# Optimization experiments

Measured on AMD Instinct MI355X. Metric: run time of the kernel, lower is better.

Reference implementation:

```python
import jax, jax.numpy as jnp
import numpy as np

NUM_USERS = 100000
NUM_ITEMS = 20000
DIM = 64
NUM_TAG = 64
NUM_NEG = 8
B = 262144
M_IMP = 2000
MARGIN1 = 0.1
MARGIN2 = 0.1
LAMBDA1 = 1.0
LAMBDA2 = 1.0
TAU = 0.2
EPS = 1e-7
MAX_NORM = 1.0 - 1e-5


def _norm(x, keepdims=True):
    return jnp.sqrt(jnp.maximum(jnp.sum(x * x, -1, keepdims=keepdims), 1e-15))


def artanh(x):
    x = jnp.clip(x, -MAX_NORM, MAX_NORM)
    return 0.5 * (jnp.log1p(x) - jnp.log1p(-x))


def acosh(z):
    z = jnp.maximum(z, 1.0 + EPS)
    return jnp.log(z + jnp.sqrt(z * z - 1.0))


# ---- Poincare ball, c = 1 ----
def ball_projx(x):
    n = _norm(x)
    return jnp.where(n > MAX_NORM, x * (MAX_NORM / n), x)


def ball_expmap0(u):
    n = _norm(u)
    return jnp.tanh(n) * u / n


def ball_logmap0(x):
    n = _norm(x)
    return artanh(n) * x / n


def mobius_add(x, y):
    xy = jnp.sum(x * y, -1, keepdims=True)
    x2 = jnp.sum(x * x, -1, keepdims=True)
    y2 = jnp.sum(y * y, -1, keepdims=True)
    num = (1.0 + 2.0 * xy + y2) * x + (1.0 - x2) * y
    den = 1.0 + 2.0 * xy + x2 * y2
    return num / jnp.maximum(den, 1e-15)


def mobius_matvec(w, x):
    # x: [..., in], w: [out, in] -> mx = x @ w.T (geoopt convention)
    mx = x @ w.T
    xn = _norm(x)
    mn = _norm(mx)
    return jnp.tanh(mn / xn * artanh(xn)) * mx / mn


def ball_dist2(x, y):
    d = 2.0 * artanh(_norm(mobius_add(-x, y), keepdims=False))
    return d * d


# ---- Lorentz, k = 1 ----
def lorentz_dist2(x, y):
    inner = jnp.sum(x[..., 1:] * y[..., 1:], -1) - x[..., 0] * y[..., 0]
    d = acosh(-inner)
    return d * d


def setup_inputs() -> dict:
    key = jax.random.key(0)
    ks = jax.random.split(key, 10)
    # Lorentz points (k=1): x0 = sqrt(1 + ||x_spatial||^2)
    sp = jax.random.normal(ks[0], (NUM_USERS + NUM_ITEMS, DIM - 1), jnp.float32) * 0.5
    t = jnp.sqrt(1.0 + jnp.sum(sp * sp, -1, keepdims=True))
    embeddings = jnp.concatenate([t, sp], -1)
    vtg_weight = jax.random.normal(ks[1], (NUM_ITEMS, DIM), jnp.float32) * 0.01
    emb_tag = ball_expmap0(jax.random.normal(ks[2], (NUM_TAG, DIM), jnp.float32) * 0.1)
    kk = (6.0 / (2 * DIM)) ** 0.5
    lin_weight = jax.random.uniform(ks[3], (DIM, DIM), jnp.float32, -kk, kk)
    lin_bias = ball_expmap0(jax.random.normal(ks[4], (DIM,), jnp.float32) * 0.001)
    tag_weight = jnp.zeros((NUM_TAG,), jnp.float32)
    uu = jax.random.randint(ks[5], (B, 1), 0, NUM_USERS)
    it = jax.random.randint(ks[6], (B, 1 + NUM_NEG), NUM_USERS, NUM_USERS + NUM_ITEMS)
    triples = jnp.concatenate([uu, it], 1)
    tag_labels = jax.random.randint(ks[7], (NUM_ITEMS, NUM_TAG), 0, 2)
    a = jax.random.randint(ks[8], (M_IMP,), 0, NUM_TAG)
    b = (a + 1 + jax.random.randint(ks[9], (M_IMP,), 0, NUM_TAG - 1)) % NUM_TAG
    implication = jnp.stack([a, b], 1)
    return dict(embeddings=embeddings, vtg_weight=vtg_weight, emb_tag=emb_tag,
                lin_weight=lin_weight, lin_bias=lin_bias, tag_weight=tag_weight,
                triples=triples, tag_labels=tag_labels, implication=implication)


def reference(embeddings, vtg_weight, emb_tag, lin_weight, lin_bias, tag_weight,
              triples, tag_labels, implication):
    # ---- hyperbolic margin-ranking loss ----
    u = embeddings[triples[:, 0]]                         # [B, D]
    pos = embeddings[triples[:, 1]]                       # [B, D]
    neg = embeddings[triples[:, 2:]]                      # [B, NEG, D]
    pos_scores = lorentz_dist2(u, pos)[:, None]           # [B, 1]
    neg_scores = lorentz_dist2(u[:, None, :], neg)        # [B, NEG]
    # alpha = sqrt(dist2(u, origin)) = acosh(u0) for Lorentz k=1
    alpha = acosh(u[:, 0])[:, None]
    rank_loss = jnp.sum(jnp.maximum((pos_scores - neg_scores + MARGIN2) * alpha, 0.0))

    # ---- Ex_loss: MobiusLinear then tangent-space cdist ----
    enc = ball_projx(vtg_weight)
    h = mobius_matvec(lin_weight, enc)
    h = ball_projx(mobius_add(h, lin_bias[None, :]))
    a = ball_logmap0(h)                                   # [I, D]
    bt = ball_logmap0(emb_tag)                            # [T, D]
    sq = jnp.sum(a * a, -1)[:, None] + jnp.sum(bt * bt, -1)[None, :] - 2.0 * a @ bt.T
    dist = jnp.sqrt(jnp.maximum(sq, 1e-12))
    logits = dist / jnp.exp(tag_weight)[None, :]          # [I, T]
    logp = jnp.log(logits)
    # relu(log(target) - log(all_dist) + margin1) summed over all tags,
    # masked to the positive-tag positions (== np.where(tag_labels>0) gather)
    term = jnp.maximum(logp[:, :, None] - logp[:, None, :] + MARGIN1, 0.0)  # [I, T, T]
    mask = (tag_labels > 0).astype(logp.dtype)
    cls_loss = jnp.sum(term.sum(-1) * mask)

    # ---- tag-hierarchy contrastive loss ----
    q = emb_tag[implication[:, 0]]
    p = emb_tag[implication[:, 1]]
    dist_pos = ball_dist2(q, p)[:, None]                               # [M, 1]
    dist_neg = ball_dist2(q[:, None, :], emb_tag[None, :, :])          # [M, T]
    full = jnp.concatenate([dist_pos, dist_neg], 1)                    # [M, T+1]
    # original filters out entries <= 1e-9 (the self-distance zero); masking
    # them to -inf in logit space is the permutation-invariant equivalent
    cl_logits = jnp.where(full > 1e-9, -full / TAU, -1e30)
    cl_loss = jnp.sum(jax.nn.logsumexp(cl_logits, axis=1) + dist_pos[:, 0] / TAU)

    return rank_loss + LAMBDA1 * cls_loss + LAMBDA2 * cl_loss
```

## Files before the change

### kernel.cpp

```cpp
#include <hip/hip_runtime.h>
#include <math.h>

namespace {

constexpr int NUM_NEG   = 8;
constexpr int BROWS     = 262144;
constexpr float MARGIN1 = 0.1f;
constexpr float MARGIN2 = 0.1f;
constexpr float TAU     = 0.2f;
constexpr float EPS1    = 1e-7f;
constexpr float MAXNORM = 1.0f - 1e-5f;

constexpr int RANK_BLOCKS = 4096;
constexpr int RANK_WAVES  = RANK_BLOCKS * 4;
constexpr int CLS_BLOCKS  = 2500;
constexpr int CLS_WAVES   = CLS_BLOCKS * 4;
constexpr int CL_BLOCKS   = 500;
constexpr int NBLK = RANK_BLOCKS + CLS_BLOCKS + CL_BLOCKS;

typedef __attribute__((ext_vector_type(4))) float f32x4;

__device__ __forceinline__ float wredsum(float v) {
    v += __shfl_xor(v, 1);  v += __shfl_xor(v, 2);  v += __shfl_xor(v, 4);
    v += __shfl_xor(v, 8);  v += __shfl_xor(v, 16); v += __shfl_xor(v, 32);
    return v;
}
__device__ __forceinline__ void wredsum2(float& a, float& b) {
    a += __shfl_xor(a, 1);  b += __shfl_xor(b, 1);
    a += __shfl_xor(a, 2);  b += __shfl_xor(b, 2);
    a += __shfl_xor(a, 4);  b += __shfl_xor(b, 4);
    a += __shfl_xor(a, 8);  b += __shfl_xor(b, 8);
    a += __shfl_xor(a, 16); b += __shfl_xor(b, 16);
    a += __shfl_xor(a, 32); b += __shfl_xor(b, 32);
}
__device__ __forceinline__ void wredsum4(float& a, float& b, float& c, float& d) {
    a += __shfl_xor(a, 1);  b += __shfl_xor(b, 1);
    c += __shfl_xor(c, 1);  d += __shfl_xor(d, 1);
    a += __shfl_xor(a, 2);  b += __shfl_xor(b, 2);
    c += __shfl_xor(c, 2);  d += __shfl_xor(d, 2);
    a += __shfl_xor(a, 4);  b += __shfl_xor(b, 4);
    c += __shfl_xor(c, 4);  d += __shfl_xor(d, 4);
    a += __shfl_xor(a, 8);  b += __shfl_xor(b, 8);
    c += __shfl_xor(c, 8);  d += __shfl_xor(d, 8);
    a += __shfl_xor(a, 16); b += __shfl_xor(b, 16);
    c += __shfl_xor(c, 16); d += __shfl_xor(d, 16);
    a += __shfl_xor(a, 32); b += __shfl_xor(b, 32);
    c += __shfl_xor(c, 32); d += __shfl_xor(d, 32);
}
__device__ __forceinline__ float wredmax(float v) {
    v = fmaxf(v, __shfl_xor(v, 1));  v = fmaxf(v, __shfl_xor(v, 2));
    v = fmaxf(v, __shfl_xor(v, 4));  v = fmaxf(v, __shfl_xor(v, 8));
    v = fmaxf(v, __shfl_xor(v, 16)); v = fmaxf(v, __shfl_xor(v, 32));
    return v;
}
__device__ __forceinline__ float bcast(float v, int l) {
    return __int_as_float(__builtin_amdgcn_readlane(__float_as_int(v), l));
}
__device__ __forceinline__ float fsq(float x)  { return __builtin_amdgcn_sqrtf(x); }
__device__ __forceinline__ float frc(float x)  { return __builtin_amdgcn_rcpf(x); }
__device__ __forceinline__ float artanh_fast(float n) {
    n = fminf(n, MAXNORM);
    return 0.5f * __logf((1.f + n) * frc(1.f - n));
}
__device__ __forceinline__ float acosh_fast(float z) {
    z = fmaxf(z, 1.0f + EPS1);
    return __logf(z + fsq(fmaf(z, z, -1.0f)));
}
__device__ __forceinline__ float tanh_fast(float x) {
    const float t = __expf(2.f * x);
    return (t - 1.f) * frc(t + 1.f);
}
__device__ __forceinline__ float dot4(const f32x4& a, const f32x4& b) {
    return (a.x * b.x + a.y * b.y) + (a.z * b.z + a.w * b.w);
}

__global__ __launch_bounds__(256) void fused_kernel(
        const float* __restrict__ emb,  const int* __restrict__ tri,
        const float* __restrict__ vtg,  const float* __restrict__ etag,
        const float* __restrict__ linw, const float* __restrict__ linb,
        const float* __restrict__ tw,   const int* __restrict__ labels,
        const int* __restrict__ imp,    float* __restrict__ part) {
    __shared__ float SA[64 * 65];
    __shared__ float XS[4 * 128];
    __shared__ float s64v[64];
    __shared__ float red4[4];
    const int tid  = threadIdx.x;
    const int lane = tid & 63, wid = tid >> 6;
    const int b    = blockIdx.x;
    float wsum = 0.f;

    const int rb  = (int)(((long)b       * RANK_BLOCKS) / NBLK);
    const int rb1 = (int)(((long)(b + 1) * RANK_BLOCKS) / NBLK);
    const bool is_rank = (rb1 > rb);
    const int  o = b - rb;

    if (is_rank) {
        const int gw  = rb * 4 + wid;
        const int sub = lane & 7;
        const int rw  = lane >> 3;
        const int dof = sub * 8;
        const bool o0 = sub & 1;
        const bool o1 = (sub >> 1) & 1;
        const bool o2 = (sub >> 2) & 1;
        float racc = 0.f;

        const int  row0 = gw * 8 + rw;
        const int* t0 = tri + (long)row0 * 10;
        const int* t1 = t0 + (long)(RANK_WAVES * 8) * 10;
        const int2 a01 = *reinterpret_cast<const int2*>(t0);
        const int2 a23 = *reinterpret_cast<const int2*>(t0 + 2);
        const int2 a45 = *reinterpret_cast<const int2*>(t0 + 4);
        const int2 a67 = *reinterpret_cast<const int2*>(t0 + 6);
        const int2 a89 = *reinterpret_cast<const int2*>(t0 + 8);
        const int2 b01 = *reinterpret_cast<const int2*>(t1);
        const int2 b23 = *reinterpret_cast<const int2*>(t1 + 2);
        const int2 b45 = *reinterpret_cast<const int2*>(t1 + 4);
        const int2 b67 = *reinterpret_cast<const int2*>(t1 + 6);
        const int2 b89 = *reinterpret_cast<const int2*>(t1 + 8);

        auto ldvec = [&](int idx, f32x4& lo, f32x4& hi) {
            const float* q = emb + (long)idx * 64 + dof;
            lo = *reinterpret_cast<const f32x4*>(q);
            hi = *reinterpret_cast<const f32x4*>(q + 4);
        };
        auto finish = [&](float e0, float e1, float e2, float e3,
                          float e4, float e5, float e6, float e7,
                          float ps, float alpha) {
            float s_;
            s_ = o0 ? e0 : e1; s_ = __shfl_xor(s_, 1); const float f0 = (o0 ? e1 : e0) + s_;
            s_ = o0 ? e2 : e3; s_ = __shfl_xor(s_, 1); const float f1 = (o0 ? e3 : e2) + s_;
            s_ = o0 ? e4 : e5; s_ = __shfl_xor(s_, 1); const float f2 = (o0 ? e5 : e4) + s_;
            s_ = o0 ? e6 : e7; s_ = __shfl_xor(s_, 1); const float f3 = (o0 ? e7 : e6) + s_;
            s_ = o1 ? f0 : f1; s_ = __shfl_xor(s_, 2); const float g0 = (o1 ? f1 : f0) + s_;
            s_ = o1 ? f2 : f3; s_ = __shfl_xor(s_, 2); const float g1 = (o1 ? f3 : f2) + s_;
            s_ = o2 ? g0 : g1; s_ = __shfl_xor(s_, 4); const float dn = (o2 ? g1 : g0) + s_;
            const float dneg = acosh_fast(-dn);
            racc += alpha * fmaxf(ps - dneg * dneg + MARGIN2, 0.f);
        };

        f32x4 ua0, ub0, pa0, pb0;
        f32x4 na0,nb0, na1,nb1, na2,nb2, na3,nb3, na4,nb4, na5,nb5, na6,nb6, na7,nb7;
        ldvec(a01.x, ua0, ub0);  ldvec(a01.y, pa0, pb0);
        ldvec(a23.x, na0, nb0);  ldvec(a23.y, na1, nb1);
        ldvec(a45.x, na2, nb2);  ldvec(a45.y, na3, nb3);
        ldvec(a67.x, na4, nb4);  ldvec(a67.y, na5, nb5);
        ldvec(a89.x, na6, nb6);  ldvec(a89.y, na7, nb7);
        asm volatile(""
            : "+v"(ua0), "+v"(ub0), "+v"(pa0), "+v"(pb0),
              "+v"(na0), "+v"(nb0), "+v"(na1), "+v"(nb1),
              "+v"(na2), "+v"(nb2), "+v"(na3), "+v"(nb3),
              "+v"(na4), "+v"(nb4), "+v"(na5), "+v"(nb5),
              "+v"(na6), "+v"(nb6), "+v"(na7), "+v"(nb7));

        const float u00  = ua0.x;
        const float u0b0 = __shfl(u00, lane & 56);
        if (sub == 0) ua0.x = -ua0.x;
        float dp0 = dot4(ua0, pa0) + dot4(ub0, pb0);
        dp0 += __shfl_xor(dp0, 1); dp0 += __shfl_xor(dp0, 2); dp0 += __shfl_xor(dp0, 4);
        const float dpos0  = acosh_fast(-dp0);
        const float ps0    = dpos0 * dpos0;
        const float alpha0 = acosh_fast(u0b0);
        const float e0 = dot4(ua0, na0) + dot4(ub0, nb0);
        const float e1 = dot4(ua0, na1) + dot4(ub0, nb1);
        const float e2 = dot4(ua0, na2) + dot4(ub0, nb2);
        const float e3 = dot4(ua0, na3) + dot4(ub0, nb3);
        const float e4 = dot4(ua0, na4) + dot4(ub0, nb4);
        const float e5 = dot4(ua0, na5) + dot4(ub0, nb5);
        const float e6 = dot4(ua0, na6) + dot4(ub0, nb6);
        const float e7 = dot4(ua0, na7) + dot4(ub0, nb7);
        finish(e0, e1, e2, e3, e4, e5, e6, e7, ps0, alpha0);

        f32x4 ua1, ub1, pa1, pb1;
        f32x4 qa0,qb0, qa1,qb1, qa2,qb2, qa3,qb3, qa4,qb4, qa5,qb5, qa6,qb6, qa7,qb7;
        ldvec(b01.x, ua1, ub1);  ldvec(b01.y, pa1, pb1);
        ldvec(b23.x, qa0, qb0);  ldvec(b23.y, qa1, qb1);
        ldvec(b45.x, qa2, qb2);  ldvec(b45.y, qa3, qb3);
        ldvec(b67.x, qa4, qb4);  ldvec(b67.y, qa5, qb5);
        ldvec(b89.x, qa6, qb6);  ldvec(b89.y, qa7, qb7);
        asm volatile(""
            : "+v"(ua1), "+v"(ub1), "+v"(pa1), "+v"(pb1),
              "+v"(qa0), "+v"(qb0), "+v"(qa1), "+v"(qb1),
              "+v"(qa2), "+v"(qb2), "+v"(qa3), "+v"(qb3),
              "+v"(qa4), "+v"(qb4), "+v"(qa5), "+v"(qb5),
              "+v"(qa6), "+v"(qb6), "+v"(qa7), "+v"(qb7));

        const float u01  = ua1.x;
        const float u0b1 = __shfl(u01, lane & 56);
        if (sub == 0) ua1.x = -ua1.x;
        float dp1 = dot4(ua1, pa1) + dot4(ub1, pb1);
        dp1 += __shfl_xor(dp1, 1); dp1 += __shfl_xor(dp1, 2); dp1 += __shfl_xor(dp1, 4);
        const float dpos1  = acosh_fast(-dp1);
        const float ps1    = dpos1 * dpos1;
        const float alpha1 = acosh_fast(u0b1);
        const float h0 = dot4(ua1, qa0) + dot4(ub1, qb0);
        const float h1 = dot4(ua1, qa1) + dot4(ub1, qb1);
        const float h2 = dot4(ua1, qa2) + dot4(ub1, qb2);
        const float h3 = dot4(ua1, qa3) + dot4(ub1, qb3);
        const float h4 = dot4(ua1, qa4) + dot4(ub1, qb4);
        const float h5 = dot4(ua1, qa5) + dot4(ub1, qb5);
        const float h6 = dot4(ua1, qa6) + dot4(ub1, qb6);
        const float h7 = dot4(ua1, qa7) + dot4(ub1, qb7);
        finish(h0, h1, h2, h3, h4, h5, h6, h7, ps1, alpha1);

        wsum = wredsum(racc);
    } else if (o < CLS_BLOCKS) {
        const int gw = o * 4 + wid;
        const int i0 = gw, i1 = gw + CLS_WAVES;
        const int xb = wid * 128;

        for (int i = tid; i < 4096; i += 256) {
            SA[(i & 63) * 65 + (i >> 6)] = linw[i];
        }
        __syncthreads();
        const float bias = linb[lane];
        const float y2b  = wredsum(bias * bias);

        float xv0 = vtg[(long)i0 * 64 + lane];
        float xv1 = vtg[(long)i1 * 64 + lane];
        float n20 = xv0 * xv0, n21 = xv1 * xv1;
        wredsum2(n20, n21);
        float xn0 = fsq(fmaxf(n20, 1e-15f)), xn1 = fsq(fmaxf(n21, 1e-15f));
        if (xn0 > MAXNORM) { xv0 *= MAXNORM * frc(xn0); float t = wredsum(xv0 * xv0); xn0 = fsq(fmaxf(t, 1e-15f)); }
        if (xn1 > MAXNORM) { xv1 *= MAXNORM * frc(xn1); float t = wredsum(xv1 * xv1); xn1 = fsq(fmaxf(t, 1e-15f)); }

        XS[xb + lane]      = xv0;
        XS[xb + 64 + lane] = xv1;
        float ma0 = 0.f, ma1 = 0.f, mb0 = 0.f, mb1 = 0.f;
        #pragma unroll
        for (int d = 0; d < 64; d += 2) {
            const float w0 = SA[(d)     * 65 + lane];
            const float w1 = SA[(d + 1) * 65 + lane];
            const float xA0 = XS[xb + d],      xA1 = XS[xb + d + 1];
            const float xB0 = XS[xb + 64 + d], xB1 = XS[xb + 64 + d + 1];
            ma0 = fmaf(xA0, w0, ma0);  ma1 = fmaf(xA1, w1, ma1);
            mb0 = fmaf(xB0, w0, mb0);  mb1 = fmaf(xB1, w1, mb1);
        }
        const float mxA = ma0 + ma1, mxB = mb0 + mb1;

        float mnA2 = mxA * mxA, mnB2 = mxB * mxB;
        wredsum2(mnA2, mnB2);
        const float mnA = fsq(fmaxf(mnA2, 1e-15f)), mnB = fsq(fmaxf(mnB2, 1e-15f));
        const float gA = tanh_fast(mnA * frc(xn0) * artanh_fast(xn0));
        const float gB = tanh_fast(mnB * frc(xn1) * artanh_fast(xn1));
        const float hA = gA * frc(mnA) * mxA, hB = gB * frc(mnB) * mxB;
        float x2hA = hA * hA, xyA = hA * bias, x2hB = hB * hB, xyB = hB * bias;
        wredsum4(x2hA, xyA, x2hB, xyB);
        const float AA  = 1.f + 2.f * xyA + y2b, AB = 1.f + 2.f * xyB + y2b;
        const float BcA = 1.f - x2hA,            BcB = 1.f - x2hB;
        const float denA = fmaxf(1.f + 2.f * xyA + x2hA * y2b, 1e-15f);
        const float denB = fmaxf(1.f + 2.f * xyB + x2hB * y2b, 1e-15f);
        float hhA = (AA * hA + BcA * bias) * frc(denA);
        float hhB = (AB * hB + BcB * bias) * frc(denB);
        float h2A = hhA * hhA, h2B = hhB * hhB;
        wredsum2(h2A, h2B);
        float hnA = fsq(fmaxf(h2A, 1e-15f)), hnB = fsq(fmaxf(h2B, 1e-15f));
        if (hnA > MAXNORM) { hhA *= MAXNORM * frc(hnA); float t = wredsum(hhA * hhA); hnA = fsq(fmaxf(t, 1e-15f)); }
        if (hnB > MAXNORM) { hhB *= MAXNORM * frc(hnB); float t = wredsum(hhB * hhB); hnB = fsq(fmaxf(t, 1e-15f)); }
        const float aA = artanh_fast(hnA) * frc(hnA) * hhA;
        const float aB = artanh_fast(hnB) * frc(hnB) * hhB;

        XS[xb + lane]      = aA;
        XS[xb + 64 + lane] = aB;
        __syncthreads();
        {
            const int j = tid >> 2, p = tid & 3;
            float e[16]; float s2 = 0.f;
            #pragma unroll
            for (int m = 0; m < 16; ++m) { e[m] = etag[j * 64 + p * 16 + m]; s2 += e[m] * e[m]; }
            s2 += __shfl_xor(s2, 1); s2 += __shfl_xor(s2, 2);
            const float n  = fsq(fmaxf(s2, 1e-15f));
            const float sc = artanh_fast(n) * frc(n);
            #pragma unroll
            for (int m = 0; m < 16; ++m) SA[(p * 16 + m) * 65 + j] = sc * e[m];
            if (p == 0) s64v[j] = sc * sc * s2;
        }
        __syncthreads();

        float da0 = 0.f, da1 = 0.f, db0 = 0.f, db1 = 0.f;
        #pragma unroll
        for (int d = 0; d < 64; d += 2) {
            const float w0 = SA[(d)     * 65 + lane];
            const float w1 = SA[(d + 1) * 65 + lane];
            const float xA0 = XS[xb + d],      xA1 = XS[xb + d + 1];
            const float xB0 = XS[xb + 64 + d], xB1 = XS[xb + 64 + d + 1];
            da0 = fmaf(xA0, w0, da0);  da1 = fmaf(xA1, w1, da1);
            db0 = fmaf(xB0, w0, db0);  db1 = fmaf(xB1, w1, db1);
        }
        float a2A = aA * aA, a2B = aB * aB;
        wredsum2(a2A, a2B);
        const float b2l = s64v[lane];
        const float twl = tw[lane];
        const float distA = fsq(fmaxf(a2A + b2l - 2.f * (da0 + da1), 1e-12f));
        const float distB = fsq(fmaxf(a2B + b2l - 2.f * (db0 + db1), 1e-12f));
        const float lpA = __logf(distA) - twl;
        const float lpB = __logf(distB) - twl;

        XS[xb + lane]      = lpA;
        XS[xb + 64 + lane] = lpB;
        const float qA = lpA + MARGIN1, qB = lpB + MARGIN1;
        float s00 = 0.f, s01 = 0.f, s10 = 0.f, s11 = 0.f;
        #pragma unroll
        for (int k = 0; k < 64; k += 2) {
            const float lA0 = XS[xb + k],      lA1 = XS[xb + k + 1];
            const float lB0 = XS[xb + 64 + k], lB1 = XS[xb + 64 + k + 1];
            s00 += fmaxf(qA - lA0, 0.f);  s01 += fmaxf(qA - lA1, 0.f);
            s10 += fmaxf(qB - lB0, 0.f);  s11 += fmaxf(qB - lB1, 0.f);
        }
        const float hsA = s00 + s01, hsB = s10 + s11;
        const float cA = (labels[(long)i0 * 64 + lane] > 0) ? hsA : 0.f;
        const float cB = (labels[(long)i1 * 64 + lane] > 0) ? hsB : 0.f;
        wsum = wredsum(cA + cB);
    } else {
        const int gw = (o - CLS_BLOCKS) * 4 + wid;
        {
            const int j = tid >> 2, p = tid & 3;
            float s2 = 0.f;
            #pragma unroll
            for (int m = 0; m < 16; ++m) {
                const float e = etag[j * 64 + p * 16 + m];
                s2 += e * e;
                SA[(p * 16 + m) * 65 + j] = e;
            }
            s2 += __shfl_xor(s2, 1); s2 += __shfl_xor(s2, 2);
            if (p == 0) s64v[j] = s2;
        }
        __syncthreads();
        const int ai = imp[gw * 2];
        const int bi = imp[gw * 2 + 1];
        const float y2l = s64v[lane];
        const float x2  = s64v[ai];
        float c0 = 0.f, c1 = 0.f, c2 = 0.f, c3 = 0.f;
        #pragma unroll
        for (int d = 0; d < 64; d += 4) {
            c0 = fmaf(SA[(d)     * 65 + ai], SA[(d)     * 65 + lane], c0);
            c1 = fmaf(SA[(d + 1) * 65 + ai], SA[(d + 1) * 65 + lane], c1);
            c2 = fmaf(SA[(d + 2) * 65 + ai], SA[(d + 2) * 65 + lane], c2);
            c3 = fmaf(SA[(d + 3) * 65 + ai], SA[(d + 3) * 65 + lane], c3);
        }
        const float c   = (c0 + c1) + (c2 + c3);
        const float A   = 1.f - 2.f * c + y2l;
        const float Bc  = 1.f - x2;
        const float nn  = A * A * x2 - 2.f * A * Bc * c + Bc * Bc * y2l;
        const float den = fmaxf(1.f - 2.f * c + x2 * y2l, 1e-15f);
        float n = fsq(fmaxf(nn * frc(den * den), 1e-15f));
        n = fminf(n, MAXNORM);
        const float dd = __logf((1.f + n) * frc(1.f - n));
        float dist = dd * dd;
        if (lane == ai) dist = 0.f;
        const float logit = (dist > 1e-9f) ? (-dist * (1.f / TAU)) : -1e30f;
        const float dp = bcast(dist, bi);
        const float lp = bcast(logit, bi);
        const float m  = wredmax(logit);
        const float se = wredsum(__expf(logit - m)) + __expf(lp - m);
        wsum = m + __logf(se) + dp * (1.f / TAU);
    }

    if (lane == 0) red4[wid] = wsum;
    __syncthreads();
    if (tid == 0) part[b] = red4[0] + red4[1] + red4[2] + red4[3];
}

__global__ __launch_bounds__(256) void final_reduce(
        const float* __restrict__ parts, int n, float* __restrict__ out) {
    __shared__ double red[256];
    double s = 0.0;
    for (int i = threadIdx.x; i < n; i += 256) s += (double)parts[i];
    red[threadIdx.x] = s;
    __syncthreads();
    for (int off = 128; off > 0; off >>= 1) {
        if (threadIdx.x < off) red[threadIdx.x] += red[threadIdx.x + off];
        __syncthreads();
    }
    if (threadIdx.x == 0) out[0] = (float)red[0];
}

}

extern "C" void kernel_launch(void* const* d_in, const int* in_sizes, int n_in,
                              void* d_out, int out_size, void* d_ws, size_t ws_size,
                              hipStream_t stream) {
    const float* emb    = (const float*)d_in[0];
    const float* vtg    = (const float*)d_in[1];
    const float* etag   = (const float*)d_in[2];
    const float* linw   = (const float*)d_in[3];
    const float* linb   = (const float*)d_in[4];
    const float* tw     = (const float*)d_in[5];
    const int*   tri    = (const int*)d_in[6];
    const int*   labels = (const int*)d_in[7];
    const int*   imp    = (const int*)d_in[8];
    float* parts = (float*)d_ws;

    fused_kernel<<<NBLK, 256, 0, stream>>>(emb, tri, vtg, etag, linw, linb,
                                           tw, labels, imp, parts);
    final_reduce<<<1, 256, 0, stream>>>(parts, NBLK, (float*)d_out);
}
```

Baseline: 72.22 us.

## Cut grid size fourfold with per-wave loops over more rows in each branch

Shrinks the rank, classification and contrastive block counts by a factor of four. Each wave now loops over 8 rank rows (instead of 2), 8 item rows (instead of 2) and 4 implication pairs (instead of 1). This amortizes per-block setup, such as loading weight matrices into shared memory and the tag tables, and reduces the number of partial sums. The cost is fewer blocks, which means less parallelism and latency hiding for the gather-heavy rank section, plus a longer serial dependency chain per wave.

```diff
diff --git a/kernel.cpp b/kernel.cpp
--- a/kernel.cpp
+++ b/kernel.cpp
@@ -11,11 +11,13 @@
 constexpr float EPS1    = 1e-7f;
 constexpr float MAXNORM = 1.0f - 1e-5f;
 
-constexpr int RANK_BLOCKS = 4096;
+constexpr int RANK_BLOCKS = 1024;
 constexpr int RANK_WAVES  = RANK_BLOCKS * 4;
-constexpr int CLS_BLOCKS  = 2500;
+constexpr int RANK_SWEEPS = 8;
+constexpr int CLS_BLOCKS  = 625;
 constexpr int CLS_WAVES   = CLS_BLOCKS * 4;
-constexpr int CL_BLOCKS   = 500;
+constexpr int CL_BLOCKS   = 125;
+constexpr int CL_WAVES    = CL_BLOCKS * 4;
 constexpr int NBLK = RANK_BLOCKS + CLS_BLOCKS + CL_BLOCKS;
 
 typedef __attribute__((ext_vector_type(4))) float f32x4;
@@ -102,30 +104,55 @@
         const bool o0 = sub & 1;
         const bool o1 = (sub >> 1) & 1;
         const bool o2 = (sub >> 2) & 1;
+        const int row0 = gw * 8 + rw;
         float racc = 0.f;
-
-        const int  row0 = gw * 8 + rw;
-        const int* t0 = tri + (long)row0 * 10;
-        const int* t1 = t0 + (long)(RANK_WAVES * 8) * 10;
-        const int2 a01 = *reinterpret_cast<const int2*>(t0);
-        const int2 a23 = *reinterpret_cast<const int2*>(t0 + 2);
-        const int2 a45 = *reinterpret_cast<const int2*>(t0 + 4);
-        const int2 a67 = *reinterpret_cast<const int2*>(t0 + 6);
-        const int2 a89 = *reinterpret_cast<const int2*>(t0 + 8);
-        const int2 b01 = *reinterpret_cast<const int2*>(t1);
-        const int2 b23 = *reinterpret_cast<const int2*>(t1 + 2);
-        const int2 b45 = *reinterpret_cast<const int2*>(t1 + 4);
-        const int2 b67 = *reinterpret_cast<const int2*>(t1 + 6);
-        const int2 b89 = *reinterpret_cast<const int2*>(t1 + 8);
 
         auto ldvec = [&](int idx, f32x4& lo, f32x4& hi) {
             const float* q = emb + (long)idx * 64 + dof;
             lo = *reinterpret_cast<const f32x4*>(q);
             hi = *reinterpret_cast<const f32x4*>(q + 4);
         };
-        auto finish = [&](float e0, float e1, float e2, float e3,
-                          float e4, float e5, float e6, float e7,
-                          float ps, float alpha) {
+
+        #pragma unroll 2
+        for (int s = 0; s < RANK_SWEEPS; ++s) {
+            const int* t = tri + (long)(row0 + s * (RANK_WAVES * 8)) * 10;
+            const int2 a01 = *reinterpret_cast<const int2*>(t);
+            const int2 a23 = *reinterpret_cast<const int2*>(t + 2);
+            const int2 a45 = *reinterpret_cast<const int2*>(t + 4);
+            const int2 a67 = *reinterpret_cast<const int2*>(t + 6);
+            const int2 a89 = *reinterpret_cast<const int2*>(t + 8);
+
+            f32x4 ua, ub, pa, pb;
+            f32x4 na0,nb0, na1,nb1, na2,nb2, na3,nb3,
+                  na4,nb4, na5,nb5, na6,nb6, na7,nb7;
+            ldvec(a01.x, ua, ub);    ldvec(a01.y, pa, pb);
+            ldvec(a23.x, na0, nb0);  ldvec(a23.y, na1, nb1);
+            ldvec(a45.x, na2, nb2);  ldvec(a45.y, na3, nb3);
+            ldvec(a67.x, na4, nb4);  ldvec(a67.y, na5, nb5);
+            ldvec(a89.x, na6, nb6);  ldvec(a89.y, na7, nb7);
+            asm volatile(""
+                : "+v"(ua), "+v"(ub), "+v"(pa), "+v"(pb),
+                  "+v"(na0), "+v"(nb0), "+v"(na1), "+v"(nb1),
+                  "+v"(na2), "+v"(nb2), "+v"(na3), "+v"(nb3),
+                  "+v"(na4), "+v"(nb4), "+v"(na5), "+v"(nb5),
+                  "+v"(na6), "+v"(nb6), "+v"(na7), "+v"(nb7));
+
+            const float u0  = ua.x;
+            const float u0b = __shfl(u0, lane & 56);
+            if (sub == 0) ua.x = -ua.x;
+            float dp = dot4(ua, pa) + dot4(ub, pb);
+            dp += __shfl_xor(dp, 1); dp += __shfl_xor(dp, 2); dp += __shfl_xor(dp, 4);
+            const float dpos  = acosh_fast(-dp);
+            const float ps    = dpos * dpos;
+            const float alpha = acosh_fast(u0b);
+            const float e0 = dot4(ua, na0) + dot4(ub, nb0);
+            const float e1 = dot4(ua, na1) + dot4(ub, nb1);
+            const float e2 = dot4(ua, na2) + dot4(ub, nb2);
+            const float e3 = dot4(ua, na3) + dot4(ub, nb3);
+            const float e4 = dot4(ua, na4) + dot4(ub, nb4);
+            const float e5 = dot4(ua, na5) + dot4(ub, nb5);
+            const float e6 = dot4(ua, na6) + dot4(ub, nb6);
+            const float e7 = dot4(ua, na7) + dot4(ub, nb7);
             float s_;
             s_ = o0 ? e0 : e1; s_ = __shfl_xor(s_, 1); const float f0 = (o0 ? e1 : e0) + s_;
             s_ = o0 ? e2 : e3; s_ = __shfl_xor(s_, 1); const float f1 = (o0 ? e3 : e2) + s_;
@@ -136,76 +163,10 @@
             s_ = o2 ? g0 : g1; s_ = __shfl_xor(s_, 4); const float dn = (o2 ? g1 : g0) + s_;
             const float dneg = acosh_fast(-dn);
             racc += alpha * fmaxf(ps - dneg * dneg + MARGIN2, 0.f);
-        };
-
-        f32x4 ua0, ub0, pa0, pb0;
-        f32x4 na0,nb0, na1,nb1, na2,nb2, na3,nb3, na4,nb4, na5,nb5, na6,nb6, na7,nb7;
-        ldvec(a01.x, ua0, ub0);  ldvec(a01.y, pa0, pb0);
-        ldvec(a23.x, na0, nb0);  ldvec(a23.y, na1, nb1);
-        ldvec(a45.x, na2, nb2);  ldvec(a45.y, na3, nb3);
-        ldvec(a67.x, na4, nb4);  ldvec(a67.y, na5, nb5);
-        ldvec(a89.x, na6, nb6);  ldvec(a89.y, na7, nb7);
-        asm volatile(""
-            : "+v"(ua0), "+v"(ub0), "+v"(pa0), "+v"(pb0),
-              "+v"(na0), "+v"(nb0), "+v"(na1), "+v"(nb1),
-              "+v"(na2), "+v"(nb2), "+v"(na3), "+v"(nb3),
-              "+v"(na4), "+v"(nb4), "+v"(na5), "+v"(nb5),
-              "+v"(na6), "+v"(nb6), "+v"(na7), "+v"(nb7));
-
-        const float u00  = ua0.x;
-        const float u0b0 = __shfl(u00, lane & 56);
-        if (sub == 0) ua0.x = -ua0.x;
-        float dp0 = dot4(ua0, pa0) + dot4(ub0, pb0);
-        dp0 += __shfl_xor(dp0, 1); dp0 += __shfl_xor(dp0, 2); dp0 += __shfl_xor(dp0, 4);
-        const float dpos0  = acosh_fast(-dp0);
-        const float ps0    = dpos0 * dpos0;
-        const float alpha0 = acosh_fast(u0b0);
-        const float e0 = dot4(ua0, na0) + dot4(ub0, nb0);
-        const float e1 = dot4(ua0, na1) + dot4(ub0, nb1);
-        const float e2 = dot4(ua0, na2) + dot4(ub0, nb2);
-        const float e3 = dot4(ua0, na3) + dot4(ub0, nb3);
-        const float e4 = dot4(ua0, na4) + dot4(ub0, nb4);
-        const float e5 = dot4(ua0, na5) + dot4(ub0, nb5);
-        const float e6 = dot4(ua0, na6) + dot4(ub0, nb6);
-        const float e7 = dot4(ua0, na7) + dot4(ub0, nb7);
-        finish(e0, e1, e2, e3, e4, e5, e6, e7, ps0, alpha0);
-
-        f32x4 ua1, ub1, pa1, pb1;
-        f32x4 qa0,qb0, qa1,qb1, qa2,qb2, qa3,qb3, qa4,qb4, qa5,qb5, qa6,qb6, qa7,qb7;
-        ldvec(b01.x, ua1, ub1);  ldvec(b01.y, pa1, pb1);
-        ldvec(b23.x, qa0, qb0);  ldvec(b23.y, qa1, qb1);
-        ldvec(b45.x, qa2, qb2);  ldvec(b45.y, qa3, qb3);
-        ldvec(b67.x, qa4, qb4);  ldvec(b67.y, qa5, qb5);
-        ldvec(b89.x, qa6, qb6);  ldvec(b89.y, qa7, qb7);
-        asm volatile(""
-            : "+v"(ua1), "+v"(ub1), "+v"(pa1), "+v"(pb1),
-              "+v"(qa0), "+v"(qb0), "+v"(qa1), "+v"(qb1),
-              "+v"(qa2), "+v"(qb2), "+v"(qa3), "+v"(qb3),
-              "+v"(qa4), "+v"(qb4), "+v"(qa5), "+v"(qb5),
-              "+v"(qa6), "+v"(qb6), "+v"(qa7), "+v"(qb7));
-
-        const float u01  = ua1.x;
-        const float u0b1 = __shfl(u01, lane & 56);
-        if (sub == 0) ua1.x = -ua1.x;
-        float dp1 = dot4(ua1, pa1) + dot4(ub1, pb1);
-        dp1 += __shfl_xor(dp1, 1); dp1 += __shfl_xor(dp1, 2); dp1 += __shfl_xor(dp1, 4);
-        const float dpos1  = acosh_fast(-dp1);
-        const float ps1    = dpos1 * dpos1;
-        const float alpha1 = acosh_fast(u0b1);
-        const float h0 = dot4(ua1, qa0) + dot4(ub1, qb0);
-        const float h1 = dot4(ua1, qa1) + dot4(ub1, qb1);
-        const float h2 = dot4(ua1, qa2) + dot4(ub1, qb2);
-        const float h3 = dot4(ua1, qa3) + dot4(ub1, qb3);
-        const float h4 = dot4(ua1, qa4) + dot4(ub1, qb4);
-        const float h5 = dot4(ua1, qa5) + dot4(ub1, qb5);
-        const float h6 = dot4(ua1, qa6) + dot4(ub1, qb6);
-        const float h7 = dot4(ua1, qa7) + dot4(ub1, qb7);
-        finish(h0, h1, h2, h3, h4, h5, h6, h7, ps1, alpha1);
-
+        }
         wsum = wredsum(racc);
     } else if (o < CLS_BLOCKS) {
         const int gw = o * 4 + wid;
-        const int i0 = gw, i1 = gw + CLS_WAVES;
         const int xb = wid * 128;
 
         for (int i = tid; i < 4096; i += 256) {
@@ -215,52 +176,54 @@
         const float bias = linb[lane];
         const float y2b  = wredsum(bias * bias);
 
-        float xv0 = vtg[(long)i0 * 64 + lane];
-        float xv1 = vtg[(long)i1 * 64 + lane];
-        float n20 = xv0 * xv0, n21 = xv1 * xv1;
-        wredsum2(n20, n21);
-        float xn0 = fsq(fmaxf(n20, 1e-15f)), xn1 = fsq(fmaxf(n21, 1e-15f));
-        if (xn0 > MAXNORM) { xv0 *= MAXNORM * frc(xn0); float t = wredsum(xv0 * xv0); xn0 = fsq(fmaxf(t, 1e-15f)); }
-        if (xn1 > MAXNORM) { xv1 *= MAXNORM * frc(xn1); float t = wredsum(xv1 * xv1); xn1 = fsq(fmaxf(t, 1e-15f)); }
-
-        XS[xb + lane]      = xv0;
-        XS[xb + 64 + lane] = xv1;
-        float ma0 = 0.f, ma1 = 0.f, mb0 = 0.f, mb1 = 0.f;
-        #pragma unroll
-        for (int d = 0; d < 64; d += 2) {
-            const float w0 = SA[(d)     * 65 + lane];
-            const float w1 = SA[(d + 1) * 65 + lane];
-            const float xA0 = XS[xb + d],      xA1 = XS[xb + d + 1];
-            const float xB0 = XS[xb + 64 + d], xB1 = XS[xb + 64 + d + 1];
-            ma0 = fmaf(xA0, w0, ma0);  ma1 = fmaf(xA1, w1, ma1);
-            mb0 = fmaf(xB0, w0, mb0);  mb1 = fmaf(xB1, w1, mb1);
-        }
-        const float mxA = ma0 + ma1, mxB = mb0 + mb1;
-
-        float mnA2 = mxA * mxA, mnB2 = mxB * mxB;
-        wredsum2(mnA2, mnB2);
-        const float mnA = fsq(fmaxf(mnA2, 1e-15f)), mnB = fsq(fmaxf(mnB2, 1e-15f));
-        const float gA = tanh_fast(mnA * frc(xn0) * artanh_fast(xn0));
-        const float gB = tanh_fast(mnB * frc(xn1) * artanh_fast(xn1));
-        const float hA = gA * frc(mnA) * mxA, hB = gB * frc(mnB) * mxB;
-        float x2hA = hA * hA, xyA = hA * bias, x2hB = hB * hB, xyB = hB * bias;
-        wredsum4(x2hA, xyA, x2hB, xyB);
-        const float AA  = 1.f + 2.f * xyA + y2b, AB = 1.f + 2.f * xyB + y2b;
-        const float BcA = 1.f - x2hA,            BcB = 1.f - x2hB;
-        const float denA = fmaxf(1.f + 2.f * xyA + x2hA * y2b, 1e-15f);
-        const float denB = fmaxf(1.f + 2.f * xyB + x2hB * y2b, 1e-15f);
-        float hhA = (AA * hA + BcA * bias) * frc(denA);
-        float hhB = (AB * hB + BcB * bias) * frc(denB);
-        float h2A = hhA * hhA, h2B = hhB * hhB;
-        wredsum2(h2A, h2B);
-        float hnA = fsq(fmaxf(h2A, 1e-15f)), hnB = fsq(fmaxf(h2B, 1e-15f));
-        if (hnA > MAXNORM) { hhA *= MAXNORM * frc(hnA); float t = wredsum(hhA * hhA); hnA = fsq(fmaxf(t, 1e-15f)); }
-        if (hnB > MAXNORM) { hhB *= MAXNORM * frc(hnB); float t = wredsum(hhB * hhB); hnB = fsq(fmaxf(t, 1e-15f)); }
-        const float aA = artanh_fast(hnA) * frc(hnA) * hhA;
-        const float aB = artanh_fast(hnB) * frc(hnB) * hhB;
-
-        XS[xb + lane]      = aA;
-        XS[xb + 64 + lane] = aB;
+        auto p1pair = [&](int iA, int iB, float& outA, float& outB) {
+            float xv0 = vtg[(long)iA * 64 + lane];
+            float xv1 = vtg[(long)iB * 64 + lane];
+            float n20 = xv0 * xv0, n21 = xv1 * xv1;
+            wredsum2(n20, n21);
+            float xn0 = fsq(fmaxf(n20, 1e-15f)), xn1 = fsq(fmaxf(n21, 1e-15f));
+            if (xn0 > MAXNORM) { xv0 *= MAXNORM * frc(xn0); float t = wredsum(xv0 * xv0); xn0 = fsq(fmaxf(t, 1e-15f)); }
+            if (xn1 > MAXNORM) { xv1 *= MAXNORM * frc(xn1); float t = wredsum(xv1 * xv1); xn1 = fsq(fmaxf(t, 1e-15f)); }
+            XS[xb + lane]      = xv0;
+            XS[xb + 64 + lane] = xv1;
+            float ma0 = 0.f, ma1 = 0.f, mb0 = 0.f, mb1 = 0.f;
+            #pragma unroll
+            for (int d = 0; d < 64; d += 2) {
+                const float w0 = SA[(d)     * 65 + lane];
+                const float w1 = SA[(d + 1) * 65 + lane];
+                const float xA0 = XS[xb + d],      xA1 = XS[xb + d + 1];
+                const float xB0 = XS[xb + 64 + d], xB1 = XS[xb + 64 + d + 1];
+                ma0 = fmaf(xA0, w0, ma0);  ma1 = fmaf(xA1, w1, ma1);
+                mb0 = fmaf(xB0, w0, mb0);  mb1 = fmaf(xB1, w1, mb1);
+            }
+            const float mxA = ma0 + ma1, mxB = mb0 + mb1;
+            float mnA2 = mxA * mxA, mnB2 = mxB * mxB;
+            wredsum2(mnA2, mnB2);
+            const float mnA = fsq(fmaxf(mnA2, 1e-15f)), mnB = fsq(fmaxf(mnB2, 1e-15f));
+            const float gA = tanh_fast(mnA * frc(xn0) * artanh_fast(xn0));
+            const float gB = tanh_fast(mnB * frc(xn1) * artanh_fast(xn1));
+            const float hA = gA * frc(mnA) * mxA, hB = gB * frc(mnB) * mxB;
+            float x2hA = hA * hA, xyA = hA * bias, x2hB = hB * hB, xyB = hB * bias;
+            wredsum4(x2hA, xyA, x2hB, xyB);
+            const float AA  = 1.f + 2.f * xyA + y2b, AB = 1.f + 2.f * xyB + y2b;
+            const float BcA = 1.f - x2hA,            BcB = 1.f - x2hB;
+            const float denA = fmaxf(1.f + 2.f * xyA + x2hA * y2b, 1e-15f);
+            const float denB = fmaxf(1.f + 2.f * xyB + x2hB * y2b, 1e-15f);
+            float hhA = (AA * hA + BcA * bias) * frc(denA);
+            float hhB = (AB * hB + BcB * bias) * frc(denB);
+            float h2A = hhA * hhA, h2B = hhB * hhB;
+            wredsum2(h2A, h2B);
+            float hnA = fsq(fmaxf(h2A, 1e-15f)), hnB = fsq(fmaxf(h2B, 1e-15f));
+            if (hnA > MAXNORM) { hhA *= MAXNORM * frc(hnA); float t = wredsum(hhA * hhA); hnA = fsq(fmaxf(t, 1e-15f)); }
+            if (hnB > MAXNORM) { hhB *= MAXNORM * frc(hnB); float t = wredsum(hhB * hhB); hnB = fsq(fmaxf(t, 1e-15f)); }
+            outA = artanh_fast(hnA) * frc(hnA) * hhA;
+            outB = artanh_fast(hnB) * frc(hnB) * hhB;
+        };
+        float av0, av1, av2, av3, av4, av5, av6, av7;
+        p1pair(gw,                 gw + CLS_WAVES,     av0, av1);
+        p1pair(gw + 2 * CLS_WAVES, gw + 3 * CLS_WAVES, av2, av3);
+        p1pair(gw + 4 * CLS_WAVES, gw + 5 * CLS_WAVES, av4, av5);
+        p1pair(gw + 6 * CLS_WAVES, gw + 7 * CLS_WAVES, av6, av7);
         __syncthreads();
         {
             const int j = tid >> 2, p = tid & 3;
@@ -275,41 +238,50 @@
             if (p == 0) s64v[j] = sc * sc * s2;
         }
         __syncthreads();
-
-        float da0 = 0.f, da1 = 0.f, db0 = 0.f, db1 = 0.f;
-        #pragma unroll
-        for (int d = 0; d < 64; d += 2) {
-            const float w0 = SA[(d)     * 65 + lane];
-            const float w1 = SA[(d + 1) * 65 + lane];
-            const float xA0 = XS[xb + d],      xA1 = XS[xb + d + 1];
-            const float xB0 = XS[xb + 64 + d], xB1 = XS[xb + 64 + d + 1];
-            da0 = fmaf(xA0, w0, da0);  da1 = fmaf(xA1, w1, da1);
-            db0 = fmaf(xB0, w0, db0);  db1 = fmaf(xB1, w1, db1);
-        }
-        float a2A = aA * aA, a2B = aB * aB;
-        wredsum2(a2A, a2B);
         const float b2l = s64v[lane];
         const float twl = tw[lane];
-        const float distA = fsq(fmaxf(a2A + b2l - 2.f * (da0 + da1), 1e-12f));
-        const float distB = fsq(fmaxf(a2B + b2l - 2.f * (db0 + db1), 1e-12f));
-        const float lpA = __logf(distA) - twl;
-        const float lpB = __logf(distB) - twl;
-
-        XS[xb + lane]      = lpA;
-        XS[xb + 64 + lane] = lpB;
-        const float qA = lpA + MARGIN1, qB = lpB + MARGIN1;
-        float s00 = 0.f, s01 = 0.f, s10 = 0.f, s11 = 0.f;
-        #pragma unroll
-        for (int k = 0; k < 64; k += 2) {
-            const float lA0 = XS[xb + k],      lA1 = XS[xb + k + 1];
-            const float lB0 = XS[xb + 64 + k], lB1 = XS[xb + 64 + k + 1];
-            s00 += fmaxf(qA - lA0, 0.f);  s01 += fmaxf(qA - lA1, 0.f);
-            s10 += fmaxf(qB - lB0, 0.f);  s11 += fmaxf(qB - lB1, 0.f);
-        }
-        const float hsA = s00 + s01, hsB = s10 + s11;
-        const float cA = (labels[(long)i0 * 64 + lane] > 0) ? hsA : 0.f;
-        const float cB = (labels[(long)i1 * 64 + lane] > 0) ? hsB : 0.f;
-        wsum = wredsum(cA + cB);
+
+        auto p2pair = [&](float aA, float aB, int iA, int iB) -> float {
+            XS[xb + lane]      = aA;
+            XS[xb + 64 + lane] = aB;
+            float da0 = 0.f, da1 = 0.f, db0 = 0.f, db1 = 0.f;
+            #pragma unroll
+            for (int d = 0; d < 64; d += 2) {
+                const float w0 = SA[(d)     * 65 + lane];
+                const float w1 = SA[(d + 1) * 65 + lane];
+                const float xA0 = XS[xb + d],      xA1 = XS[xb + d + 1];
+                const float xB0 = XS[xb + 64 + d], xB1 = XS[xb + 64 + d + 1];
+                da0 = fmaf(xA0, w0, da0);  da1 = fmaf(xA1, w1, da1);
+                db0 = fmaf(xB0, w0, db0);  db1 = fmaf(xB1, w1, db1);
+            }
+            float a2A = aA * aA, a2B = aB * aB;
+            wredsum2(a2A, a2B);
+            const float distA = fsq(fmaxf(a2A + b2l - 2.f * (da0 + da1), 1e-12f));
+            const float distB = fsq(fmaxf(a2B + b2l - 2.f * (db0 + db1), 1e-12f));
+            const float lpA = __logf(distA) - twl;
+            const float lpB = __logf(distB) - twl;
+            XS[xb + lane]      = lpA;
+            XS[xb + 64 + lane] = lpB;
+            const float qA = lpA + MARGIN1, qB = lpB + MARGIN1;
+            float s00 = 0.f, s01 = 0.f, s10 = 0.f, s11 = 0.f;
+            #pragma unroll
+            for (int k = 0; k < 64; k += 2) {
+                const float lA0 = XS[xb + k],      lA1 = XS[xb + k + 1];
+                const float lB0 = XS[xb + 64 + k], lB1 = XS[xb + 64 + k + 1];
+                s00 += fmaxf(qA - lA0, 0.f);  s01 += fmaxf(qA - lA1, 0.f);
+                s10 += fmaxf(qB - lB0, 0.f);  s11 += fmaxf(qB - lB1, 0.f);
+            }
+            const float hsA = s00 + s01, hsB = s10 + s11;
+            const float cA = (labels[(long)iA * 64 + lane] > 0) ? hsA : 0.f;
+            const float cB = (labels[(long)iB * 64 + lane] > 0) ? hsB : 0.f;
+            return cA + cB;
+        };
+        float acc = 0.f;
+        acc += p2pair(av0, av1, gw,                 gw + CLS_WAVES);
+        acc += p2pair(av2, av3, gw + 2 * CLS_WAVES, gw + 3 * CLS_WAVES);
+        acc += p2pair(av4, av5, gw + 4 * CLS_WAVES, gw + 5 * CLS_WAVES);
+        acc += p2pair(av6, av7, gw + 6 * CLS_WAVES, gw + 7 * CLS_WAVES);
+        wsum = wredsum(acc);
     } else {
         const int gw = (o - CLS_BLOCKS) * 4 + wid;
         {
@@ -325,34 +297,40 @@
             if (p == 0) s64v[j] = s2;
         }
         __syncthreads();
-        const int ai = imp[gw * 2];
-        const int bi = imp[gw * 2 + 1];
         const float y2l = s64v[lane];
-        const float x2  = s64v[ai];
-        float c0 = 0.f, c1 = 0.f, c2 = 0.f, c3 = 0.f;
+        float acc = 0.f;
         #pragma unroll
-        for (int d = 0; d < 64; d += 4) {
-            c0 = fmaf(SA[(d)     * 65 + ai], SA[(d)     * 65 + lane], c0);
-            c1 = fmaf(SA[(d + 1) * 65 + ai], SA[(d + 1) * 65 + lane], c1);
-            c2 = fmaf(SA[(d + 2) * 65 + ai], SA[(d + 2) * 65 + lane], c2);
-            c3 = fmaf(SA[(d + 3) * 65 + ai], SA[(d + 3) * 65 + lane], c3);
-        }
-        const float c   = (c0 + c1) + (c2 + c3);
-        const float A   = 1.f - 2.f * c + y2l;
-        const float Bc  = 1.f - x2;
-        const float nn  = A * A * x2 - 2.f * A * Bc * c + Bc * Bc * y2l;
-        const float den = fmaxf(1.f - 2.f * c + x2 * y2l, 1e-15f);
-        float n = fsq(fmaxf(nn * frc(den * den), 1e-15f));
-        n = fminf(n, MAXNORM);
-        const float dd = __logf((1.f + n) * frc(1.f - n));
-        float dist = dd * dd;
-        if (lane == ai) dist = 0.f;
-        const float logit = (dist > 1e-9f) ? (-dist * (1.f / TAU)) : -1e30f;
-        const float dp = bcast(dist, bi);
-        const float lp = bcast(logit, bi);
-        const float m  = wredmax(logit);
-        const float se = wredsum(__expf(logit - m)) + __expf(lp - m);
-        wsum = m + __logf(se) + dp * (1.f / TAU);
+        for (int k = 0; k < 4; ++k) {
+            const int pI = gw + k * CL_WAVES;
+            const int ai = imp[pI * 2];
+            const int bi = imp[pI * 2 + 1];
+            const float x2 = s64v[ai];
+            float c0 = 0.f, c1 = 0.f, c2 = 0.f, c3 = 0.f;
+            #pragma unroll
+            for (int d = 0; d < 64; d += 4) {
+                c0 = fmaf(SA[(d)     * 65 + ai], SA[(d)     * 65 + lane], c0);
+                c1 = fmaf(SA[(d + 1) * 65 + ai], SA[(d + 1) * 65 + lane], c1);
+                c2 = fmaf(SA[(d + 2) * 65 + ai], SA[(d + 2) * 65 + lane], c2);
+                c3 = fmaf(SA[(d + 3) * 65 + ai], SA[(d + 3) * 65 + lane], c3);
+            }
+            const float c   = (c0 + c1) + (c2 + c3);
+            const float A   = 1.f - 2.f * c + y2l;
+            const float Bc  = 1.f - x2;
+            const float nn  = A * A * x2 - 2.f * A * Bc * c + Bc * Bc * y2l;
+            const float den = fmaxf(1.f - 2.f * c + x2 * y2l, 1e-15f);
+            float n = fsq(fmaxf(nn * frc(den * den), 1e-15f));
+            n = fminf(n, MAXNORM);
+            const float dd = __logf((1.f + n) * frc(1.f - n));
+            float dist = dd * dd;
+            if (lane == ai) dist = 0.f;
+            const float logit = (dist > 1e-9f) ? (-dist * (1.f / TAU)) : -1e30f;
+            const float dp = bcast(dist, bi);
+            const float lp = bcast(logit, bi);
+            const float m  = wredmax(logit);
+            const float se = wredsum(__expf(logit - m)) + __expf(lp - m);
+            acc += m + __logf(se) + dp * (1.f / TAU);
+        }
+        wsum = acc;
     }
 
     if (lane == 0) red4[wid] = wsum;
```

After: 122.4 us. 69.5% more time.
